# Performance work log

Hardware: AMD Instinct MI355X
Metric: run time of the kernel (lower is better)

## Reference

```python
import jax, jax.numpy as jnp
import numpy as np


def setup_inputs() -> dict:
    key = jax.random.key(0)
    k1, k2, k3 = jax.random.split(key, 3)
    N = 16384
    y = jax.random.normal(k1, (N,), dtype=jnp.float32)
    y_hat = jax.random.normal(k2, (N,), dtype=jnp.float32)
    status = jax.random.randint(k3, (N,), 0, 2, dtype=jnp.int32)
    return {"y": y, "y_hat": y_hat, "status": status}


def reference(y, y_hat, status):
    # Pairwise concordance index over all pairs i < j.
    # ge[i, j] = y[i] >= y[j]; le[i, j] = y[i] <= y[j]
    N = y.shape[0]
    ge = y[:, None] >= y[None, :]
    le = y[:, None] <= y[None, :]
    ge_hat = y_hat[:, None] >= y_hat[None, :]
    le_hat = y_hat[:, None] <= y_hat[None, :]
    st_i = (status == 1)[:, None]  # astatus_1 broadcast over j
    st_j = (status == 1)[None, :]  # bstatus_1 broadcast over i
    # upper-triangular mask (strict): pairs with j > i
    mask = jnp.triu(jnp.ones((N, N), dtype=bool), k=1)

    c1 = ge & ge_hat & st_j
    c2 = le & le_hat & st_i
    cc = (c1 | c2) & mask

    tp1 = le & st_i
    tp2 = ge & st_j
    tp = (tp1 | tp2) & mask

    c = jnp.sum(cc.astype(jnp.int32)).astype(jnp.float32)
    total_pairs = jnp.sum(tp.astype(jnp.int32)).astype(jnp.float32)
    return c / total_pairs
```

## Files before the change

### kernel.cpp

```cpp
#include <hip/hip_runtime.h>


#define BLOCK 256
#define GRID  1024
#define RAWJ  512
#define TI    512

__global__ __launch_bounds__(BLOCK, 4) void cindex_one(
    const float* __restrict__ y, const float* __restrict__ yh,
    const int* __restrict__ status, int n,
    unsigned* __restrict__ ws, float* __restrict__ out)
{
    __shared__ __align__(16) float2 s_yy[RAWJ];
    __shared__ unsigned s_cnt, s_jc;
    __shared__ unsigned rA[4], rB[4];
    __shared__ int s_win;

    const int tid  = threadIdx.x;
    const int b    = blockIdx.x;
    const int lane = tid & 63;
    const int wav  = tid >> 6;

    const float PINF = __int_as_float(0x7f800000);
    const float NINF = __int_as_float(0xff800000);

    const int ntJ  = (n + RAWJ - 1) / RAWJ;
    const int ntI  = (n + TI - 1) / TI;
    const int ntot = ntI * ntJ;

    unsigned bg = 0, bc = 0;

    for (int t = b; t < ntot; t += GRID) {
        const int ti = t / ntJ;
        const int tj = t - ti * ntJ;

        if (tid == 0) s_cnt = 0;
        __syncthreads();

        const int jr0 = tj * RAWJ + tid;
#pragma unroll
        for (int r = 0; r < RAWJ / BLOCK; ++r) {
            const int jr = jr0 + r * BLOCK;
            if (jr < n && status[jr] == 1) {
                unsigned p = atomicAdd(&s_cnt, 1u);
                s_yy[p] = make_float2(y[jr], yh[jr]);
            }
        }
        __syncthreads();
        if (tid < 8) {
            unsigned jc  = s_cnt;
            unsigned jcp = (jc + 7u) & ~7u;
            unsigned idx = jc + (unsigned)tid;
            if (idx < jcp) s_yy[idx] = make_float2(PINF, PINF);
            if (tid == 0) s_jc = jcp;
        }
        __syncthreads();
        const int jcnt = (int)s_jc;

        const int i0 = ti * TI + tid;
        const int i1 = i0 + BLOCK;
        const float yi0 = (i0 < n) ? y[i0]  : NINF;
        const float hh0 = (i0 < n) ? yh[i0] : NINF;
        const float yi1 = (i1 < n) ? y[i1]  : NINF;
        const float hh1 = (i1 < n) ? yh[i1] : NINF;

        for (int jj = 0; jj < jcnt; jj += 8) {
#pragma unroll
            for (int k = 0; k < 8; ++k) {
                float2 p = s_yy[jj + k];
                bool g0 = yi0 >= p.x, h0 = hh0 >= p.y;
                bool g1 = yi1 >= p.x, h1 = hh1 >= p.y;
                bg += (unsigned)g0 + (unsigned)g1;
                bc += (unsigned)(g0 & h0) + (unsigned)(g1 & h1);
            }
        }
        __syncthreads();
    }

#pragma unroll
    for (int off = 32; off > 0; off >>= 1) {
        bg += __shfl_down(bg, off, 64);
        bc += __shfl_down(bc, off, 64);
    }
    if (lane == 0) { rA[wav] = bg; rB[wav] = bc; }
    __syncthreads();

    const unsigned ref = ws[0];

    if (tid == 0) {
        unsigned tg = rA[0] + rA[1] + rA[2] + rA[3];
        unsigned tc = rB[0] + rB[1] + rB[2] + rB[3];
        atomicAdd(&ws[16  + 16 * (b & 31)], tg);
        atomicAdd(&ws[528 + 16 * (b & 31)], tc);
        __threadfence();
        unsigned old = atomicAdd(&ws[1], 1u);
        s_win = (old - ref == (unsigned)(GRID - 1)) ? 1 : 0;
    }
    __syncthreads();

    if (s_win) {
        __threadfence();
        unsigned kc = 0;
        const int4* s4 = (const int4*)status;
        const int n4 = n >> 2;
        for (int k4 = tid; k4 < n4; k4 += BLOCK) {
            int4 v = s4[k4];
            kc += (unsigned)((v.x == 1) + (v.y == 1) + (v.z == 1) + (v.w == 1));
        }
        for (int k = (n4 << 2) + tid; k < n; k += BLOCK)
            kc += (unsigned)(status[k] == 1);
#pragma unroll
        for (int off = 32; off > 0; off >>= 1) kc += __shfl_down(kc, off, 64);
        if (lane == 0) rA[wav] = kc;

        unsigned sg = 0, sc = 0;
        if (tid < 32) {
            sg = atomicAdd(&ws[16  + 16 * tid], 0u);
            sc = atomicAdd(&ws[528 + 16 * tid], 0u);
        }
#pragma unroll
        for (int off = 32; off > 0; off >>= 1) {
            sg += __shfl_down(sg, off, 64);
            sc += __shfl_down(sc, off, 64);
        }
        __syncthreads();
        if (tid == 0) {
            unsigned K  = rA[0] + rA[1] + rA[2] + rA[3];
            unsigned T1 = sg - 32u * ref;
            unsigned S1 = sc - 32u * ref;
            long long cn = (long long)S1 - (long long)K;
            long long tn = (long long)T1 - (long long)K;
            out[0] = (float)cn / (float)tn;
        }
    }
}

extern "C" void kernel_launch(void* const* d_in, const int* in_sizes, int n_in,
                              void* d_out, int out_size, void* d_ws, size_t ws_size,
                              hipStream_t stream) {
    const float* y      = (const float*)d_in[0];
    const float* y_hat  = (const float*)d_in[1];
    const int*   status = (const int*)d_in[2];
    float* out = (float*)d_out;
    int n = in_sizes[0];
    unsigned* ws = (unsigned*)d_ws;

    hipLaunchKernelGGL(cindex_one, dim3(GRID), dim3(BLOCK), 0, stream,
                       y, y_hat, status, n, ws, out);
}
```

Before: 87.91 us.

## Use two-level completion counter and fold status count into tile pass

Replaces the single global arrival counter with 32 sharded per-group counters plus a second-level counter, so the last block is found without every block contending on one atomic. The final block no longer rescans the status array; blocks with ti==0 add their per-tile status==1 counts into sharded workspace slots, and the winner sums those. This relies on the workspace holding the ref-based baseline in the new slots and on s_waitcnt ordering in place of threadfence, which risks memory-ordering correctness.

```diff
diff --git a/kernel.cpp b/kernel.cpp
--- a/kernel.cpp
+++ b/kernel.cpp
@@ -28,6 +28,8 @@
     const int ntI  = (n + TI - 1) / TI;
     const int ntot = ntI * ntJ;
 
+    const unsigned ref = ws[0];
+
     unsigned bg = 0, bc = 0;
 
     for (int t = b; t < ntot; t += GRID) {
@@ -57,6 +59,10 @@
         __syncthreads();
         const int jcnt = (int)s_jc;
 
+        if (ti == 0 && tid == 0) {
+            atomicAdd(&ws[1552 + 16 * (tj & 31)], s_cnt);
+        }
+
         const int i0 = ti * TI + tid;
         const int i1 = i0 + BLOCK;
         const float yi0 = (i0 < n) ? y[i0]  : NINF;
@@ -85,49 +91,40 @@
     if (lane == 0) { rA[wav] = bg; rB[wav] = bc; }
     __syncthreads();
 
-    const unsigned ref = ws[0];
-
     if (tid == 0) {
         unsigned tg = rA[0] + rA[1] + rA[2] + rA[3];
         unsigned tc = rB[0] + rB[1] + rB[2] + rB[3];
-        atomicAdd(&ws[16  + 16 * (b & 31)], tg);
-        atomicAdd(&ws[528 + 16 * (b & 31)], tc);
-        __threadfence();
-        unsigned old = atomicAdd(&ws[1], 1u);
-        s_win = (old - ref == (unsigned)(GRID - 1)) ? 1 : 0;
+        unsigned o1 = atomicAdd(&ws[528  + 16 * (b & 31)], tg);
+        unsigned o2 = atomicAdd(&ws[1040 + 16 * (b & 31)], tc);
+        asm volatile("" :: "v"(o1), "v"(o2));
+        asm volatile("s_waitcnt vmcnt(0)" ::: "memory");
+        int winflag = 0;
+        unsigned og = atomicAdd(&ws[16 + 16 * (b & 31)], 1u);
+        if (og - ref == (unsigned)(GRID / 32 - 1)) {
+            unsigned os = atomicAdd(&ws[2064], 1u);
+            winflag = (os - ref == 31u) ? 1 : 0;
+        }
+        s_win = winflag;
     }
     __syncthreads();
 
     if (s_win) {
-        __threadfence();
-        unsigned kc = 0;
-        const int4* s4 = (const int4*)status;
-        const int n4 = n >> 2;
-        for (int k4 = tid; k4 < n4; k4 += BLOCK) {
-            int4 v = s4[k4];
-            kc += (unsigned)((v.x == 1) + (v.y == 1) + (v.z == 1) + (v.w == 1));
-        }
-        for (int k = (n4 << 2) + tid; k < n; k += BLOCK)
-            kc += (unsigned)(status[k] == 1);
-#pragma unroll
-        for (int off = 32; off > 0; off >>= 1) kc += __shfl_down(kc, off, 64);
-        if (lane == 0) rA[wav] = kc;
-
-        unsigned sg = 0, sc = 0;
+        unsigned sg = 0, sc = 0, sk = 0;
         if (tid < 32) {
-            sg = atomicAdd(&ws[16  + 16 * tid], 0u);
-            sc = atomicAdd(&ws[528 + 16 * tid], 0u);
+            sg = atomicAdd(&ws[528  + 16 * tid], 0u);
+            sc = atomicAdd(&ws[1040 + 16 * tid], 0u);
+            sk = atomicAdd(&ws[1552 + 16 * tid], 0u);
         }
 #pragma unroll
         for (int off = 32; off > 0; off >>= 1) {
             sg += __shfl_down(sg, off, 64);
             sc += __shfl_down(sc, off, 64);
+            sk += __shfl_down(sk, off, 64);
         }
-        __syncthreads();
         if (tid == 0) {
-            unsigned K  = rA[0] + rA[1] + rA[2] + rA[3];
             unsigned T1 = sg - 32u * ref;
             unsigned S1 = sc - 32u * ref;
+            unsigned K  = sk - 32u * ref;
             long long cn = (long long)S1 - (long long)K;
             long long tn = (long long)T1 - (long long)K;
             out[0] = (float)cn / (float)tn;
```

Measured after the change: 79.57 us. 9.5% less time.
